# Optimization experiments

Hardware: AMD Instinct MI355X
Metric: run time of the kernel (lower is better)

The kernel has to match this reference:

```python
import jax, jax.numpy as jnp
import numpy as np

NUM_SAMPLES = 5      # samples per line (line_matcher_cfg)
MIN_DIST_PTS = 8.0   # min pixel spacing between samples
TOP_K = 10           # top-k candidate lines for NW matching
GRID_SIZE = 4        # desc map stride
GAP = 0.1            # NW gap penalty


def sample_line_points(line_seg):
    # line_seg: (N, 2, 2) ij endpoints -> pts (N, S, 2), valid (N, S)
    start, end = line_seg[:, 0], line_seg[:, 1]
    lengths = jnp.linalg.norm(end - start, axis=1)
    nsamp = jnp.clip(jnp.floor(lengths / MIN_DIST_PTS), 2.0, float(NUM_SAMPLES))
    k = jnp.arange(NUM_SAMPLES, dtype=line_seg.dtype)
    interval = (end - start) / (nsamp - 1.0)[:, None]          # (N, 2)
    pts = start[:, None, :] + k[None, :, None] * interval[:, None, :]
    valid = k[None, :] < nsamp[:, None]
    pts = jnp.where(valid[..., None], pts, 0.0)                # torch pads with 0
    return pts, valid


def sample_descriptors(desc, pts):
    # Faithful F.grid_sample(bilinear, zeros padding, align_corners=False) after
    # kornia normalize_pixel_coordinates ((size-1) normalization), then L2-norm.
    # desc: (1, D, H, W); pts: (P, 2) ij coords in full-res image.
    D, H, W = desc.shape[1], desc.shape[2], desc.shape[3]
    img_h, img_w = H * GRID_SIZE, W * GRID_SIZE
    xn = 2.0 * pts[:, 1] / (img_w - 1) - 1.0
    yn = 2.0 * pts[:, 0] / (img_h - 1) - 1.0
    ix = ((xn + 1.0) * W - 1.0) / 2.0   # align_corners=False unnormalize
    iy = ((yn + 1.0) * H - 1.0) / 2.0
    x0f = jnp.floor(ix); y0f = jnp.floor(iy)
    wx = ix - x0f; wy = iy - y0f
    x0 = x0f.astype(jnp.int32); y0 = y0f.astype(jnp.int32)
    img = desc[0]

    def gather(xi, yi):
        inb = ((xi >= 0) & (xi < W) & (yi >= 0) & (yi < H)).astype(img.dtype)
        xc = jnp.clip(xi, 0, W - 1); yc = jnp.clip(yi, 0, H - 1)
        return img[:, yc, xc] * inb[None, :]   # (D, P), zeros outside

    v = (gather(x0, y0) * ((1 - wx) * (1 - wy))[None]
         + gather(x0 + 1, y0) * (wx * (1 - wy))[None]
         + gather(x0, y0 + 1) * ((1 - wx) * wy)[None]
         + gather(x0 + 1, y0 + 1) * (wx * wy)[None])
    return v / jnp.linalg.norm(v, axis=0, keepdims=True)


def needleman_wunsch(scores):
    # scores: (B, n, m); sequential DP via nested lax.scan (rows, then cols)
    B, n, m = scores.shape
    s = jnp.transpose(scores, (1, 0, 2)) - GAP  # (n, B, m)

    def row_step(prev_row, srow):               # prev_row (B, m+1), srow (B, m)
        diag = prev_row[:, :-1].T                # (m, B)
        up = prev_row[:, 1:].T                   # (m, B)

        def col_step(left, xs):
            d, u, sc = xs
            cur = jnp.maximum(jnp.maximum(left, u), d + sc)
            return cur, cur

        _, cols = jax.lax.scan(col_step, jnp.zeros((B,), s.dtype), (diag, up, srow.T))
        new_row = jnp.concatenate([jnp.zeros((B, 1), s.dtype), cols.T], axis=1)
        return new_row, None

    final, _ = jax.lax.scan(row_step, jnp.zeros((B, m + 1), s.dtype), s)
    return final[:, -1]


def filter_and_match_lines(scores):
    # scores: (N, M, n, n)
    ls1 = scores.max(3); v1 = (ls1 != -1.0).astype(scores.dtype)
    ls1 = (ls1 * v1).sum(2) / v1.sum(2)
    ls2 = scores.max(2); v2 = (ls2 != -1.0).astype(scores.dtype)
    ls2 = (ls2 * v2).sum(2) / v2.sum(2)
    line_scores = (ls1 + ls2) / 2.0
    topk_lines = jnp.argsort(line_scores, axis=1)[:, -TOP_K:]          # (N, k)
    top = jnp.take_along_axis(scores, topk_lines[:, :, None, None], axis=1)
    top = jnp.concatenate([top, jnp.flip(top, axis=-1)], axis=1)       # (N, 2k, n, n)
    N, top2k, n, m = top.shape
    nw = needleman_wunsch(top.reshape(N * top2k, n, m)).reshape(N, top2k)
    matches = jnp.argmax(nw, axis=1) % (top2k // 2)
    matches = topk_lines[jnp.arange(N), matches]
    return matches, nw


def match_forward(line_seg1, line_seg2, desc1, desc2):
    N, M = line_seg1.shape[0], line_seg2.shape[0]
    pts1, val1 = sample_line_points(line_seg1)
    pts2, val2 = sample_line_points(line_seg2)
    d1 = sample_descriptors(desc1, pts1.reshape(-1, 2))   # (D, N*S)
    d2 = sample_descriptors(desc2, pts2.reshape(-1, 2))   # (D, M*S)
    scores = d1.T @ d2                                    # (N*S, M*S)
    scores = jnp.where(val1.reshape(-1)[:, None], scores, -1.0)
    scores = jnp.where(val2.reshape(-1)[None, :], scores, -1.0)
    scores = scores.reshape(N, NUM_SAMPLES, M, NUM_SAMPLES).transpose(0, 2, 1, 3)
    matches, nw = filter_and_match_lines(scores)
    # cross check
    matches2, _ = filter_and_match_lines(scores.transpose(1, 0, 3, 2))
    mutual = matches2[matches] == jnp.arange(N)
    matches = jnp.where(mutual, matches, -1)
    return matches, nw


def setup_inputs():
    key = jax.random.key(0)
    k1, k2, k3, k4 = jax.random.split(key, 4)
    N = M = 1200; D = 128; H = W = 128
    img = float(H * GRID_SIZE - 1)
    line_seg1 = jax.random.uniform(k1, (N, 2, 2), jnp.float32) * img
    line_seg2 = jax.random.uniform(k2, (M, 2, 2), jnp.float32) * img
    desc1 = jax.random.normal(k3, (1, D, H, W), jnp.float32)
    desc2 = jax.random.normal(k4, (1, D, H, W), jnp.float32)
    return {"line_seg1": line_seg1, "line_seg2": line_seg2, "desc1": desc1, "desc2": desc2}


def reference(line_seg1, line_seg2, desc1, desc2):
    return match_forward(line_seg1, line_seg2, desc1, desc2)
```

## Files before the change

kernel.cpp:

```cpp
#include <hip/hip_runtime.h>
#include <hip/hip_bf16.h>


#define NLINES 1200
#define NS 5
#define DD 128
#define HH 128
#define WW 128
#define HW (HH*WW)
#define IMGM1 511.0f
#define GAPC 0.1f
#define NPAD 1216
#define PPAD (NPAD*NS)
#define KEXT 384
#define NCH (KEXT/32)
#define NGRP (PPAD/16)

typedef __attribute__((ext_vector_type(8))) short short8;
typedef __attribute__((ext_vector_type(4))) float f32x4;

__global__ void transpose_desc(const float* __restrict__ in1, float* __restrict__ out1,
                               const float* __restrict__ in2, float* __restrict__ out2) {
    const float* in = blockIdx.z ? in2 : in1;
    float* out = blockIdx.z ? out2 : out1;
    __shared__ float t[32][132];
    int s0 = blockIdx.x * 128;
    int d0 = blockIdx.y * 32;
    int tid = threadIdx.x;
    #pragma unroll
    for (int pass = 0; pass < 4; ++pass) {
        int idx = pass * 256 + tid;
        int dr = idx >> 5, si = idx & 31;
        float4 v = *(const float4*)&in[(size_t)(d0 + dr) * HW + s0 + 4 * si];
        *(float4*)&t[dr][4 * si] = v;
    }
    __syncthreads();
    #pragma unroll
    for (int pass = 0; pass < 4; ++pass) {
        int idx = pass * 256 + tid;
        int sr = idx >> 3, di = idx & 7;
        float4 v = { t[4 * di][sr], t[4 * di + 1][sr], t[4 * di + 2][sr], t[4 * di + 3][sr] };
        *(float4*)&out[(size_t)(s0 + sr) * DD + d0 + 4 * di] = v;
    }
}

__global__ void samplepack_kernel(const float* __restrict__ lseg1, const float* __restrict__ lseg2,
                                  const float* __restrict__ tdesc1, const float* __restrict__ tdesc2,
                                  const float* __restrict__ desc1, const float* __restrict__ desc2,
                                  short* __restrict__ Aext, short* __restrict__ Bext,
                                  float* __restrict__ val1, float* __restrict__ val2,
                                  int use_t) {
    int side = blockIdx.y;
    const float* lseg = side ? lseg2 : lseg1;
    const float* tdesc = side ? tdesc2 : tdesc1;
    const float* desc = side ? desc2 : desc1;
    short* Ef = side ? Bext : Aext;
    float* valout = side ? val2 : val1;
    int arole = side ? 0 : 1;

    __shared__ float ds[16][129];
    int g = blockIdx.x;
    int t = threadIdx.x;
    int lane = t & 63, w = t >> 6;

    #pragma unroll
    for (int s = 0; s < 4; ++s) {
        int r = w * 4 + s;
        int pt = g * 16 + r;
        int line = pt / NS;
        int k = pt - line * NS;

        float sy = 0.f, sx = 0.f, ey = 0.f, ex = 0.f;
        if (line < NLINES) {
            sy = lseg[line * 4 + 0]; sx = lseg[line * 4 + 1];
            ey = lseg[line * 4 + 2]; ex = lseg[line * 4 + 3];
        }
        float dy = ey - sy, dx = ex - sx;
        float len = sqrtf(dy * dy + dx * dx);
        float ns = floorf(len * 0.125f);
        ns = fminf(fmaxf(ns, 2.0f), 5.0f);
        float kf = (float)k;
        float validf = (kf < ns) ? 1.0f : 0.0f;
        float py = sy + kf * (dy / (ns - 1.0f));
        float px = sx + kf * (dx / (ns - 1.0f));
        if (validf == 0.0f) { py = 0.0f; px = 0.0f; }

        float xn = 2.0f * px / IMGM1 - 1.0f;
        float yn = 2.0f * py / IMGM1 - 1.0f;
        float ix = ((xn + 1.0f) * (float)WW - 1.0f) * 0.5f;
        float iy = ((yn + 1.0f) * (float)HH - 1.0f) * 0.5f;
        float x0f = floorf(ix), y0f = floorf(iy);
        float wx = ix - x0f, wy = iy - y0f;
        int x0 = (int)x0f, y0 = (int)y0f;

        float w00 = (1.0f - wx) * (1.0f - wy);
        float w10 = wx * (1.0f - wy);
        float w01 = (1.0f - wx) * wy;
        float w11 = wx * wy;

        float v0 = 0.0f, v1 = 0.0f;
        int xs[4] = { x0, x0 + 1, x0,     x0 + 1 };
        int ys[4] = { y0, y0,     y0 + 1, y0 + 1 };
        float ws4[4] = { w00, w10, w01, w11 };
        #pragma unroll
        for (int c = 0; c < 4; ++c) {
            int xi = xs[c], yi = ys[c];
            float inb = (xi >= 0 && xi < WW && yi >= 0 && yi < HH) ? 1.0f : 0.0f;
            int xc = min(max(xi, 0), WW - 1);
            int yc = min(max(yi, 0), HH - 1);
            if (use_t) {
                int base = (yc * WW + xc) * DD;
                v0 += tdesc[base + lane] * inb * ws4[c];
                v1 += tdesc[base + 64 + lane] * inb * ws4[c];
            } else {
                int base = yc * WW + xc;
                v0 += desc[lane * HW + base] * inb * ws4[c];
                v1 += desc[(lane + 64) * HW + base] * inb * ws4[c];
            }
        }
        float ss = v0 * v0 + v1 * v1;
        #pragma unroll
        for (int o = 32; o > 0; o >>= 1) ss += __shfl_xor(ss, o);
        if (ss == 0.0f) ss = 1.0f;
        float nrm = sqrtf(ss);
        ds[r][lane] = v0 / nrm;
        ds[r][64 + lane] = v1 / nrm;
        if (lane == 0) valout[pt] = (line < NLINES) ? validf : 0.0f;
    }
    __syncthreads();

    #pragma unroll
    for (int it = 0; it < 3; ++it) {
        int idx = it * 256 + t;
        int c = idx >> 6, l = idx & 63;
        int q = l >> 4, r = l & 15;
        short8 outv;
        #pragma unroll
        for (int jj = 0; jj < 8; ++jj) {
            int kext = c * 32 + q * 8 + jj;
            int term = kext >> 7, k = kext & 127;
            float x = ds[r][k];
            __hip_bfloat16 h = __float2bfloat16(x);
            short v = *(short*)&h;
            bool lo_term = arole ? (term == 1) : (term == 2);
            if (lo_term) {
                float hf = __bfloat162float(h);
                __hip_bfloat16 lw = __float2bfloat16(x - hf);
                v = *(short*)&lw;
            }
            outv[jj] = v;
        }
        *(short8*)&Ef[((size_t)(g * NCH + c) * 64 + l) * 8] = outv;
    }
}

__launch_bounds__(256, 2)
__global__ void score_kernel(const short* __restrict__ Af, const short* __restrict__ Bf,
                             const float* __restrict__ val1, const float* __restrict__ val2,
                             float* __restrict__ lsc, float* __restrict__ lscT) {
    __shared__ float dump[80 * 161];
    __shared__ float red[16][33];

    const int t = threadIdx.x;
    const int lane = t & 63;
    const int w = t >> 6;
    const int wm = w >> 1;
    const int wn = w & 1;
    const int gA0 = blockIdx.x * 10;
    const int gB0 = blockIdx.y * 10;

    const short* pa[5];
    const short* pb[5];
    #pragma unroll
    for (int ti = 0; ti < 5; ++ti) {
        pa[ti] = Af + ((size_t)(gA0 + 5 * wm + ti) * NCH * 64 + lane) * 8;
        pb[ti] = Bf + ((size_t)(gB0 + 5 * wn + ti) * NCH * 64 + lane) * 8;
    }

    f32x4 acc[5][5];
    #pragma unroll
    for (int a = 0; a < 5; ++a)
        #pragma unroll
        for (int b = 0; b < 5; ++b)
            acc[a][b] = (f32x4){0.f, 0.f, 0.f, 0.f};

    short8 ca[5], cb[5], na[5], nb[5];
    #pragma unroll
    for (int ti = 0; ti < 5; ++ti) {
        ca[ti] = *(const short8*)(pa[ti]);
        cb[ti] = *(const short8*)(pb[ti]);
    }
    #pragma unroll
    for (int c = 0; c < NCH; c += 2) {
        #pragma unroll
        for (int ti = 0; ti < 5; ++ti) {
            na[ti] = *(const short8*)(pa[ti] + (c + 1) * 512);
            nb[ti] = *(const short8*)(pb[ti] + (c + 1) * 512);
        }
        #pragma unroll
        for (int ti = 0; ti < 5; ++ti)
            #pragma unroll
            for (int tj = 0; tj < 5; ++tj)
                acc[ti][tj] = __builtin_amdgcn_mfma_f32_16x16x32_bf16(
                    ca[ti], cb[tj], acc[ti][tj], 0, 0, 0);
        if (c + 2 < NCH) {
            #pragma unroll
            for (int ti = 0; ti < 5; ++ti) {
                ca[ti] = *(const short8*)(pa[ti] + (c + 2) * 512);
                cb[ti] = *(const short8*)(pb[ti] + (c + 2) * 512);
            }
        }
        #pragma unroll
        for (int ti = 0; ti < 5; ++ti)
            #pragma unroll
            for (int tj = 0; tj < 5; ++tj)
                acc[ti][tj] = __builtin_amdgcn_mfma_f32_16x16x32_bf16(
                    na[ti], nb[tj], acc[ti][tj], 0, 0, 0);
    }

    const int i0l = blockIdx.x * 32;
    const int j0l = blockIdx.y * 32;
    #pragma unroll
    for (int p = 0; p < 2; ++p) {
        __syncthreads();
        if (wm == p) {
            #pragma unroll
            for (int ti = 0; ti < 5; ++ti) {
                #pragma unroll
                for (int reg = 0; reg < 4; ++reg) {
                    int rloc = 16 * ti + (lane >> 4) * 4 + reg;
                    #pragma unroll
                    for (int tj = 0; tj < 5; ++tj) {
                        int col = 80 * wn + 16 * tj + (lane & 15);
                        dump[rloc * 161 + col] = acc[ti][tj][reg];
                    }
                }
            }
        }
        __syncthreads();
        #pragma unroll
        for (int e = 0; e < 2; ++e) {
            int q = t * 2 + e;
            int li = q >> 5, lj = q & 31;
            int i = i0l + 16 * p + li;
            int j = j0l + lj;
            float S[5][5];
            #pragma unroll
            for (int a = 0; a < 5; ++a) {
                float va = val1[i * NS + a];
                #pragma unroll
                for (int b = 0; b < 5; ++b) {
                    float vb = val2[j * NS + b];
                    float sc = dump[(li * 5 + a) * 161 + (lj * 5 + b)];
                    S[a][b] = (va != 0.0f && vb != 0.0f) ? sc : -1.0f;
                }
            }
            float sum1 = 0.0f, cnt1 = 0.0f;
            #pragma unroll
            for (int a = 0; a < 5; ++a) {
                float r = S[a][0];
                #pragma unroll
                for (int b = 1; b < 5; ++b) r = fmaxf(r, S[a][b]);
                float v = (r != -1.0f) ? 1.0f : 0.0f;
                sum1 += r * v; cnt1 += v;
            }
            float sum2 = 0.0f, cnt2 = 0.0f;
            #pragma unroll
            for (int b = 0; b < 5; ++b) {
                float r = S[0][b];
                #pragma unroll
                for (int a = 1; a < 5; ++a) r = fmaxf(r, S[a][b]);
                float v = (r != -1.0f) ? 1.0f : 0.0f;
                sum2 += r * v; cnt2 += v;
            }
            float res = (sum1 / cnt1 + sum2 / cnt2) * 0.5f;
            red[li][lj] = res;
            if (i < NLINES && j < NLINES) lsc[i * NLINES + j] = res;
        }
        __syncthreads();
        #pragma unroll
        for (int e = 0; e < 2; ++e) {
            int q = t + 256 * e;
            int li = q & 15, lj = q >> 4;
            int i = i0l + 16 * p + li;
            int j = j0l + lj;
            if (i < NLINES && j < NLINES) lscT[j * NLINES + i] = red[li][lj];
        }
    }
}

__global__ void topk_kernel(const float* __restrict__ lsc, const float* __restrict__ lscT,
                            int* __restrict__ topk1, int* __restrict__ topk2) {
    __shared__ float wv[4];
    __shared__ int wi[4];
    int rb = blockIdx.x;
    const float* ls = (rb < NLINES) ? (lsc + rb * NLINES) : (lscT + (rb - NLINES) * NLINES);
    int* topk = (rb < NLINES) ? (topk1 + rb * 10) : (topk2 + (rb - NLINES) * 10);
    int t = threadIdx.x;
    int lane = t & 63, w = t >> 6;
    float val[5];
    #pragma unroll
    for (int s = 0; s < 5; ++s) {
        int j = t + 256 * s;
        val[s] = (j < NLINES) ? ls[j] : -1e30f;
    }
    float bv = -1e30f; int bi = -1;
    #pragma unroll
    for (int s = 0; s < 5; ++s) {
        int j = t + 256 * s;
        if (val[s] >= bv) { bv = val[s]; bi = j; }
    }
    for (int sel = 0; sel < 10; ++sel) {
        float rv = bv; int ri = bi;
        #pragma unroll
        for (int o = 32; o > 0; o >>= 1) {
            float ov = __shfl_xor(rv, o);
            int oi = __shfl_xor(ri, o);
            if (ov > rv || (ov == rv && oi > ri)) { rv = ov; ri = oi; }
        }
        if (lane == 0) { wv[w] = rv; wi[w] = ri; }
        __syncthreads();
        float fv = wv[0]; int fi = wi[0];
        #pragma unroll
        for (int qq = 1; qq < 4; ++qq)
            if (wv[qq] > fv || (wv[qq] == fv && wi[qq] > fi)) { fv = wv[qq]; fi = wi[qq]; }
        if (t == 0) topk[9 - sel] = fi;
        if ((fi & 255) == t) {
            val[fi >> 8] = -1e30f;
            bv = -1e30f; bi = -1;
            #pragma unroll
            for (int s = 0; s < 5; ++s) {
                int j = t + 256 * s;
                if (val[s] >= bv) { bv = val[s]; bi = j; }
            }
        }
        __syncthreads();
    }
}

__device__ __forceinline__ float nw5(const float* M) {
    float F[6] = {0, 0, 0, 0, 0, 0};
    #pragma unroll
    for (int x = 0; x < 5; ++x) {
        float diag = F[0];
        float left = 0.0f;
        #pragma unroll
        for (int y = 1; y <= 5; ++y) {
            float up = F[y];
            float cur = fmaxf(fmaxf(left, up), diag + (M[x * 5 + y - 1] - GAPC));
            F[y] = cur; left = cur; diag = up;
        }
    }
    return F[5];
}

__global__ void nw_kernel(const short* __restrict__ Af, const short* __restrict__ Bf,
                          const float* __restrict__ val1, const float* __restrict__ val2,
                          const int* __restrict__ topk1, const int* __restrict__ topk2,
                          float* __restrict__ nwout, float* __restrict__ nw2buf) {
    __shared__ float sbuf[10][25];
    __shared__ int jl[10];
    int rb = blockIdx.x;
    int dir = (rb >= NLINES) ? 1 : 0;
    int row = rb - dir * NLINES;
    int t = threadIdx.x;
    int w = t >> 6;
    int lane = t & 63;
    int q = lane >> 4, rr = lane & 15;

    if (t < 10) jl[t] = (dir ? topk2 : topk1)[row * 10 + t];
    __syncthreads();

    const short* shEf = dir ? Bf : Af;
    const short* cdEf = dir ? Af : Bf;

    int ptS = row * 5 + min(rr, 4);
    const short* shp = shEf + ((size_t)(ptS >> 4) * NCH * 64 + q * 16 + (ptS & 15)) * 8;

    int c1 = jl[2 * w], c2 = jl[2 * w + 1];
    int ptC = (rr < 8) ? (c1 * 5 + min(rr, 4)) : (c2 * 5 + min(rr - 8, 4));
    const short* cp = cdEf + ((size_t)(ptC >> 4) * NCH * 64 + q * 16 + (ptC & 15)) * 8;

    f32x4 acc = (f32x4){0.f, 0.f, 0.f, 0.f};
    #pragma unroll
    for (int c = 0; c < NCH; ++c) {
        short8 sh = *(const short8*)(shp + c * 512);
        short8 cb = *(const short8*)(cp + c * 512);
        acc = dir ? __builtin_amdgcn_mfma_f32_16x16x32_bf16(cb, sh, acc, 0, 0, 0)
                  : __builtin_amdgcn_mfma_f32_16x16x32_bf16(sh, cb, acc, 0, 0, 0);
    }
    #pragma unroll
    for (int reg = 0; reg < 4; ++reg) {
        int m = q * 4 + reg, n = rr;
        if (!dir) {
            if (m < 5 && n < 5) sbuf[2 * w][m * 5 + n] = acc[reg];
            if (m < 5 && n >= 8 && n < 13) sbuf[2 * w + 1][m * 5 + (n - 8)] = acc[reg];
        } else {
            if (m < 5 && n < 5) sbuf[2 * w][m * 5 + n] = acc[reg];
            if (m >= 8 && m < 13 && n < 5) sbuf[2 * w + 1][(m - 8) * 5 + n] = acc[reg];
        }
    }
    __syncthreads();

    if (t < 20) {
        int r = t >> 1, rev = t & 1;
        int i = dir ? jl[r] : row;
        int j = dir ? row : jl[r];
        float S[25];
        #pragma unroll
        for (int a = 0; a < 5; ++a) {
            float va = val1[i * NS + a];
            #pragma unroll
            for (int b = 0; b < 5; ++b) {
                float vb = val2[j * NS + b];
                S[a * 5 + b] = (va != 0.0f && vb != 0.0f) ? sbuf[r][a * 5 + b] : -1.0f;
            }
        }
        float M[25];
        #pragma unroll
        for (int x = 0; x < 5; ++x)
            #pragma unroll
            for (int y = 0; y < 5; ++y) {
                if (!dir) M[x * 5 + y] = rev ? S[x * 5 + (4 - y)] : S[x * 5 + y];
                else      M[x * 5 + y] = rev ? S[(4 - y) * 5 + x] : S[y * 5 + x];
            }
        float nwv = nw5(M);
        float* o = dir ? nw2buf : nwout;
        o[row * 20 + rev * 10 + r] = nwv;
    }
}

__global__ void argmax_final_kernel(const float* __restrict__ nw1, const float* __restrict__ nw2,
                                    const int* __restrict__ topk1, const int* __restrict__ topk2,
                                    float* __restrict__ out) {
    __shared__ int mpre[NLINES];
    __shared__ int m2[NLINES];
    int t = threadIdx.x;
    for (int qq = t; qq < 2 * NLINES; qq += 1024) {
        int dir = qq / NLINES, row = qq - dir * NLINES;
        const float* nw = (dir ? nw2 : nw1) + row * 20;
        float best = nw[0]; int bi = 0;
        #pragma unroll
        for (int q = 1; q < 20; ++q) {
            float v = nw[q];
            if (v > best) { best = v; bi = q; }
        }
        int m = (dir ? topk2 : topk1)[row * 10 + (bi % 10)];
        if (dir) m2[row] = m; else mpre[row] = m;
    }
    __syncthreads();
    for (int i = t; i < NLINES; i += 1024) {
        int m = mpre[i];
        out[i] = (m2[m] == i) ? (float)m : -1.0f;
    }
}

extern "C" void kernel_launch(void* const* d_in, const int* in_sizes, int n_in,
                              void* d_out, int out_size, void* d_ws, size_t ws_size,
                              hipStream_t stream) {
    const float* lseg1 = (const float*)d_in[0];
    const float* lseg2 = (const float*)d_in[1];
    const float* desc1 = (const float*)d_in[2];
    const float* desc2 = (const float*)d_in[3];
    float* out = (float*)d_out;

    float* wsf = (float*)d_ws;
    size_t off = 0;
    float* val1 = wsf + off;   off += PPAD;
    float* val2 = wsf + off;   off += PPAD;
    float* lsc = wsf + off;    off += (size_t)NLINES * NLINES;
    float* lscT = wsf + off;   off += (size_t)NLINES * NLINES;
    int* topk1 = (int*)(wsf + off); off += NLINES * 10;
    int* topk2 = (int*)(wsf + off); off += NLINES * 10;
    float* nw2buf = wsf + off; off += NLINES * 20;
    short* Aext = (short*)(wsf + off); off += (size_t)PPAD * KEXT / 2;
    short* Bext = (short*)(wsf + off); off += (size_t)PPAD * KEXT / 2;
    float* tdesc1 = wsf + off; off += (size_t)HW * DD;
    float* tdesc2 = wsf + off; off += (size_t)HW * DD;
    size_t need_full = off * sizeof(float);
    int use_t = (ws_size >= need_full) ? 1 : 0;

    if (use_t) {
        transpose_desc<<<dim3(HW / 128, DD / 32, 2), 256, 0, stream>>>(
            desc1, tdesc1, desc2, tdesc2);
    }
    samplepack_kernel<<<dim3(NGRP, 2), 256, 0, stream>>>(
        lseg1, lseg2, tdesc1, tdesc2, desc1, desc2, Aext, Bext, val1, val2, use_t);

    score_kernel<<<dim3(NPAD / 32, NPAD / 32), 256, 0, stream>>>(Aext, Bext, val1, val2,
                                                                 lsc, lscT);

    topk_kernel<<<2 * NLINES, 256, 0, stream>>>(lsc, lscT, topk1, topk2);

    nw_kernel<<<2 * NLINES, 320, 0, stream>>>(Aext, Bext, val1, val2, topk1, topk2,
                                              out + NLINES, nw2buf);

    argmax_final_kernel<<<1, 1024, 0, stream>>>(out + NLINES, nw2buf, topk1, topk2, out);
}
```

Baseline: 183.0 us.

## Fuse top-k selection into NW kernel and stage shared descriptors in LDS

Merges the separate top-k kernel into the NW kernel, so each block (now 320 threads, 5 waves) selects its own top-10 candidates and writes them straight to shared memory. This removes a kernel launch and the global round-trip of the topk indices. The fused kernel also prefetches the row's own descriptor fragments into LDS before the top-k loop, hiding global latency behind the selection. The cost is more shared memory per block and a top-k using 5 waves with modulo-320 indexing.

After: 182.9 us. Within noise of the previous version (-0.1%).

```diff
diff --git a/kernel.cpp b/kernel.cpp
--- a/kernel.cpp
+++ b/kernel.cpp
@@ -289,55 +289,6 @@
     }
 }
 
-__global__ void topk_kernel(const float* __restrict__ lsc, const float* __restrict__ lscT,
-                            int* __restrict__ topk1, int* __restrict__ topk2) {
-    __shared__ float wv[4];
-    __shared__ int wi[4];
-    int rb = blockIdx.x;
-    const float* ls = (rb < NLINES) ? (lsc + rb * NLINES) : (lscT + (rb - NLINES) * NLINES);
-    int* topk = (rb < NLINES) ? (topk1 + rb * 10) : (topk2 + (rb - NLINES) * 10);
-    int t = threadIdx.x;
-    int lane = t & 63, w = t >> 6;
-    float val[5];
-    #pragma unroll
-    for (int s = 0; s < 5; ++s) {
-        int j = t + 256 * s;
-        val[s] = (j < NLINES) ? ls[j] : -1e30f;
-    }
-    float bv = -1e30f; int bi = -1;
-    #pragma unroll
-    for (int s = 0; s < 5; ++s) {
-        int j = t + 256 * s;
-        if (val[s] >= bv) { bv = val[s]; bi = j; }
-    }
-    for (int sel = 0; sel < 10; ++sel) {
-        float rv = bv; int ri = bi;
-        #pragma unroll
-        for (int o = 32; o > 0; o >>= 1) {
-            float ov = __shfl_xor(rv, o);
-            int oi = __shfl_xor(ri, o);
-            if (ov > rv || (ov == rv && oi > ri)) { rv = ov; ri = oi; }
-        }
-        if (lane == 0) { wv[w] = rv; wi[w] = ri; }
-        __syncthreads();
-        float fv = wv[0]; int fi = wi[0];
-        #pragma unroll
-        for (int qq = 1; qq < 4; ++qq)
-            if (wv[qq] > fv || (wv[qq] == fv && wi[qq] > fi)) { fv = wv[qq]; fi = wi[qq]; }
-        if (t == 0) topk[9 - sel] = fi;
-        if ((fi & 255) == t) {
-            val[fi >> 8] = -1e30f;
-            bv = -1e30f; bi = -1;
-            #pragma unroll
-            for (int s = 0; s < 5; ++s) {
-                int j = t + 256 * s;
-                if (val[s] >= bv) { bv = val[s]; bi = j; }
-            }
-        }
-        __syncthreads();
-    }
-}
-
 __device__ __forceinline__ float nw5(const float* M) {
     float F[6] = {0, 0, 0, 0, 0, 0};
     #pragma unroll
@@ -354,12 +305,16 @@
     return F[5];
 }
 
-__global__ void nw_kernel(const short* __restrict__ Af, const short* __restrict__ Bf,
-                          const float* __restrict__ val1, const float* __restrict__ val2,
-                          const int* __restrict__ topk1, const int* __restrict__ topk2,
-                          float* __restrict__ nwout, float* __restrict__ nw2buf) {
+__global__ void topk_nw_kernel(const float* __restrict__ lsc, const float* __restrict__ lscT,
+                               const short* __restrict__ Af, const short* __restrict__ Bf,
+                               const float* __restrict__ val1, const float* __restrict__ val2,
+                               int* __restrict__ topk1, int* __restrict__ topk2,
+                               float* __restrict__ nwout, float* __restrict__ nw2buf) {
+    __shared__ short sh_lds[NCH * 512];
     __shared__ float sbuf[10][25];
     __shared__ int jl[10];
+    __shared__ float wv[5];
+    __shared__ int wi[5];
     int rb = blockIdx.x;
     int dir = (rb >= NLINES) ? 1 : 0;
     int row = rb - dir * NLINES;
@@ -368,14 +323,58 @@
     int lane = t & 63;
     int q = lane >> 4, rr = lane & 15;
 
-    if (t < 10) jl[t] = (dir ? topk2 : topk1)[row * 10 + t];
-    __syncthreads();
-
     const short* shEf = dir ? Bf : Af;
     const short* cdEf = dir ? Af : Bf;
-
-    int ptS = row * 5 + min(rr, 4);
-    const short* shp = shEf + ((size_t)(ptS >> 4) * NCH * 64 + q * 16 + (ptS & 15)) * 8;
+    const float* ls = dir ? (lscT + (size_t)row * NLINES) : (lsc + (size_t)row * NLINES);
+    int* topk = dir ? (topk2 + row * 10) : (topk1 + row * 10);
+
+    for (int idx = t; idx < NCH * 64; idx += 320) {
+        int c = idx >> 6, l = idx & 63;
+        int lq = l >> 4, lr = l & 15;
+        int ptS = row * 5 + min(lr, 4);
+        const short* gp = shEf + ((size_t)(ptS >> 4) * NCH * 64 + lq * 16 + (ptS & 15)) * 8
+                               + (size_t)c * 512;
+        *(short8*)&sh_lds[c * 512 + l * 8] = *(const short8*)gp;
+    }
+
+    float val[4];
+    #pragma unroll
+    for (int s = 0; s < 4; ++s) {
+        int j = t + 320 * s;
+        val[s] = (j < NLINES) ? ls[j] : -1e30f;
+    }
+    float bv = -1e30f; int bi = -1;
+    #pragma unroll
+    for (int s = 0; s < 4; ++s) {
+        int j = t + 320 * s;
+        if (val[s] >= bv) { bv = val[s]; bi = j; }
+    }
+    for (int sel = 0; sel < 10; ++sel) {
+        float rv = bv; int ri = bi;
+        #pragma unroll
+        for (int o = 32; o > 0; o >>= 1) {
+            float ov = __shfl_xor(rv, o);
+            int oi = __shfl_xor(ri, o);
+            if (ov > rv || (ov == rv && oi > ri)) { rv = ov; ri = oi; }
+        }
+        if (lane == 0) { wv[w] = rv; wi[w] = ri; }
+        __syncthreads();
+        float fv = wv[0]; int fi = wi[0];
+        #pragma unroll
+        for (int qq = 1; qq < 5; ++qq)
+            if (wv[qq] > fv || (wv[qq] == fv && wi[qq] > fi)) { fv = wv[qq]; fi = wi[qq]; }
+        if (t == 0) { topk[9 - sel] = fi; jl[9 - sel] = fi; }
+        if (fi >= 0 && (fi % 320) == t) {
+            val[fi / 320] = -1e30f;
+            bv = -1e30f; bi = -1;
+            #pragma unroll
+            for (int s = 0; s < 4; ++s) {
+                int j = t + 320 * s;
+                if (val[s] >= bv) { bv = val[s]; bi = j; }
+            }
+        }
+        __syncthreads();
+    }
 
     int c1 = jl[2 * w], c2 = jl[2 * w + 1];
     int ptC = (rr < 8) ? (c1 * 5 + min(rr, 4)) : (c2 * 5 + min(rr - 8, 4));
@@ -384,7 +383,7 @@
     f32x4 acc = (f32x4){0.f, 0.f, 0.f, 0.f};
     #pragma unroll
     for (int c = 0; c < NCH; ++c) {
-        short8 sh = *(const short8*)(shp + c * 512);
+        short8 sh = *(const short8*)&sh_lds[c * 512 + lane * 8];
         short8 cb = *(const short8*)(cp + c * 512);
         acc = dir ? __builtin_amdgcn_mfma_f32_16x16x32_bf16(cb, sh, acc, 0, 0, 0)
                   : __builtin_amdgcn_mfma_f32_16x16x32_bf16(sh, cb, acc, 0, 0, 0);
@@ -490,10 +489,8 @@
     score_kernel<<<dim3(NPAD / 32, NPAD / 32), 256, 0, stream>>>(Aext, Bext, val1, val2,
                                                                  lsc, lscT);
 
-    topk_kernel<<<2 * NLINES, 256, 0, stream>>>(lsc, lscT, topk1, topk2);
-
-    nw_kernel<<<2 * NLINES, 320, 0, stream>>>(Aext, Bext, val1, val2, topk1, topk2,
-                                              out + NLINES, nw2buf);
+    topk_nw_kernel<<<2 * NLINES, 320, 0, stream>>>(lsc, lscT, Aext, Bext, val1, val2,
+                                                   topk1, topk2, out + NLINES, nw2buf);
 
     argmax_final_kernel<<<1, 1024, 0, stream>>>(out + NLINES, nw2buf, topk1, topk2, out);
 }
```
